# Kernel tuning notes

Hardware: AMD Instinct MI355X
Metric: run time of the kernel (lower is better)

Reference implementation:

```python
import jax, jax.numpy as jnp
import numpy as np

HEADS = 12
HEAD_SIZE = 64
INF = 1e12  # K.infinity() in bert4keras

B, L, D = 8, 1024, 768


def setup_inputs() -> dict:
    key = jax.random.key(0)
    k1, k2 = jax.random.split(key)
    x = jax.random.normal(k1, (B, L, D), dtype=jnp.float32)
    W = jax.random.normal(k2, (D, HEADS * HEAD_SIZE * 2), dtype=jnp.float32) * (1.0 / np.sqrt(D))
    b = jnp.zeros((HEADS * HEAD_SIZE * 2,), dtype=jnp.float32)
    mask = jnp.ones((B, L), dtype=jnp.int32)
    return {"x": x, "W": W, "b": b, "mask": mask}


def _rope_sin_cos(seq_len, head_size, dtype):
    # SinusoidalPositionEmbedding(head_size, 'zero'):
    # emb[n, 2i] = sin(n * 10000^(-2i/S)), emb[n, 2i+1] = cos(...)
    pos = jnp.arange(seq_len, dtype=dtype)                       # [L]
    inv = jnp.power(jnp.asarray(10000.0, dtype),
                    -2.0 * jnp.arange(head_size // 2, dtype=dtype) / head_size)  # [S/2]
    ang = pos[:, None] * inv[None, :]                            # [L, S/2]
    # repeat_elements(..., 2, -1): [c0,c0,c1,c1,...]
    cos_pos = jnp.repeat(jnp.cos(ang), 2, axis=-1)               # [L, S]
    sin_pos = jnp.repeat(jnp.sin(ang), 2, axis=-1)               # [L, S]
    return sin_pos[None, :, None, :], cos_pos[None, :, None, :]  # [1,L,1,S]


def _rotate_half_interleaved(t):
    # stack([-t[...,1::2], t[...,::2]], -1).reshape(t.shape)
    t2 = jnp.stack([-t[..., 1::2], t[..., ::2]], axis=-1)
    return t2.reshape(t.shape)


def reference(x, W, b, mask):
    dtype = x.dtype
    Bq, Lq, _ = x.shape
    S = HEAD_SIZE
    # dense projection + head split: [B, L, H, 2S]
    proj = (jnp.einsum('bld,de->ble', x, W) + b).reshape(Bq, Lq, HEADS, 2 * S)
    qw, kw = proj[..., :S], proj[..., S:]
    # inline RoPE (interleaved variant)
    sin_pos, cos_pos = _rope_sin_cos(Lq, S, dtype)
    qw = qw * cos_pos + _rotate_half_interleaved(qw) * sin_pos
    kw = kw * cos_pos + _rotate_half_interleaved(kw) * sin_pos
    # bilinear score: [B, H, L, L]
    logits = jnp.einsum('bmhd,bnhd->bhmn', qw, kw)
    # padding mask on axis 2 (rows) and axis 3 (cols): x*m + (-INF)*(1-m)
    m = mask.astype(dtype)
    m_row = m[:, None, :, None]
    m_col = m[:, None, None, :]
    logits = logits * m_row + (-INF) * (1.0 - m_row)
    logits = logits * m_col + (-INF) * (1.0 - m_col)
    # upper-triangular (incl. diagonal) mask
    tri = jnp.triu(jnp.ones((Lq, Lq), dtype=dtype))
    logits = logits - (1.0 - tri) * INF
    return logits / np.sqrt(S).astype(np.float32)
```

## Files before the change

kernel.cpp:

```cpp
#include <hip/hip_runtime.h>
#include <hip/hip_bf16.h>
#include <stdint.h>

#define NHEADS 12
#define HS 64
#define NB 8
#define NL 1024
#define ND 768
#define NE 1536
#define INFV 1000000000000.0f

typedef __bf16 bf16x8 __attribute__((ext_vector_type(8)));
typedef float f32x4 __attribute__((ext_vector_type(4)));

typedef __attribute__((address_space(1))) const unsigned int gas_uint;
typedef __attribute__((address_space(3))) unsigned int las_uint;
#define GLOAD_LDS16(g, l) __builtin_amdgcn_global_load_lds((gas_uint*)(g), (las_uint*)(l), 16, 0, 0)

__device__ __forceinline__ unsigned short f2bf(float f) {
  unsigned int u = __builtin_bit_cast(unsigned int, f);
  u += 0x7fffu + ((u >> 16) & 1u);
  return (unsigned short)(u >> 16);
}

__device__ __forceinline__ bf16x8 load_frag(const unsigned short* p) {
  uint4 v = *(const uint4*)p;
  return __builtin_bit_cast(bf16x8, v);
}

__global__ __launch_bounds__(256) void k_prep(
    const float* __restrict__ x, const float* __restrict__ W,
    unsigned short* __restrict__ xb, unsigned short* __restrict__ wt,
    float* __restrict__ cst) {
  const int blk = blockIdx.x;
  if (blk < 6144) {
    int i = blk * 256 + threadIdx.x;
    float4 v = ((const float4*)x)[i];
    ushort4 o;
    o.x = f2bf(v.x); o.y = f2bf(v.y); o.z = f2bf(v.z); o.w = f2bf(v.w);
    ((ushort4*)xb)[i] = o;
  } else if (blk < 6144 + 288) {
    __shared__ float tile[64][65];
    int t = blk - 6144;
    int te = t % 24, td = t / 24;
    int c = threadIdx.x & 63, r4 = threadIdx.x >> 6;
    #pragma unroll
    for (int rr = 0; rr < 16; rr++) {
      int row = rr * 4 + r4;
      tile[row][c] = W[(size_t)(td * 64 + row) * NE + te * 64 + c];
    }
    __syncthreads();
    #pragma unroll
    for (int rr = 0; rr < 16; rr++) {
      int row = rr * 4 + r4;
      wt[(size_t)(te * 64 + row) * ND + td * 64 + c] = f2bf(tile[c][row]);
    }
  } else {
    int t = (blk - 6432) * 256 + threadIdx.x;
    int p = t >> 5, i = t & 31;
    float inv = powf(10000.0f, -(float)i / 32.0f);
    float sv, cv;
    sincosf((float)p * inv, &sv, &cv);
    cst[(p * 32 + i) * 2 + 0] = cv;
    cst[(p * 32 + i) * 2 + 1] = sv;
  }
}

__global__ __launch_bounds__(512, 4) void k_projfill(
    const unsigned short* __restrict__ xb,
    const unsigned short* __restrict__ wt,
    const float* __restrict__ bias,
    const float* __restrict__ cst,
    unsigned short* __restrict__ qbuf, unsigned short* __restrict__ kbuf,
    const int* __restrict__ mask, float* __restrict__ out) {
  __shared__ char smem_b[49152];
  const int tid = threadIdx.x;
  const int blk = blockIdx.x;

  if (blk >= 384) {
    const int e   = blk - 384;
    const int bh  = e / 28;
    int u = e % 28;
    int tm = 1;
    #pragma unroll
    for (int kk = 0; kk < 6; kk++) if (u >= tm) { u -= tm; tm++; }
    const int tn = u;
    const int b  = bh / NHEADS;
    const int* mrow = mask + b * NL;
    const int n0 = tn * 128 + (tid & 31) * 4;
    const int row = tid >> 5;
    int4 mc = *(const int4*)&mrow[n0];
    float o0 = ((mc.x ? 0.0f : -INFV) - INFV) * 0.125f;
    float o1 = ((mc.y ? 0.0f : -INFV) - INFV) * 0.125f;
    float o2 = ((mc.z ? 0.0f : -INFV) - INFV) * 0.125f;
    float o3 = ((mc.w ? 0.0f : -INFV) - INFV) * 0.125f;
    const float oz = (-2.0f * INFV) * 0.125f;
    #pragma unroll
    for (int it = 0; it < 8; it++) {
      int m = tm * 128 + it * 16 + row;
      bool mr1 = (mrow[m] != 0);
      f32x4 o;
      o[0] = mr1 ? o0 : oz;
      o[1] = mr1 ? o1 : oz;
      o[2] = mr1 ? o2 : oz;
      o[3] = mr1 ? o3 : oz;
      __builtin_nontemporal_store(o, (f32x4*)(out + ((size_t)bh * NL + m) * NL + n0));
    }
    return;
  }

  const int xcd = blk & 7;
  const int loc = blk >> 3;
  const int mt  = xcd * 4 + loc / 12;
  const int et  = loc % 12;
  const int m0  = mt * 256;
  const int e0  = et * 128;
  const int lane = tid & 63;
  const int w    = tid >> 6;
  const int wm = w >> 2, wn = w & 3;
  const int col_l = lane & 15, rq = lane >> 4;

  unsigned int goffA[2], goffB[4];
  #pragma unroll
  for (int q = 0; q < 2; q++) {
    int p = q * 512 + tid;
    int r = p >> 3, sl = p & 7;
    goffA[q] = r * ND + (sl ^ (r & 7)) * 8;
  }
  #pragma unroll
  for (int q = 0; q < 4; q++) {
    int p = q * 512 + tid;
    int r = p >> 3, sl = p & 7;
    goffB[q] = r * ND + (sl ^ (r & 7)) * 8;
  }
  const unsigned short* gA = wt + (size_t)e0 * ND;
  const unsigned short* gB = xb + (size_t)m0 * ND;

  const int xr = col_l & 7;
  const unsigned int aRow = (unsigned)((wn * 32 + col_l) * 128);
  const unsigned int bRow = (unsigned)(16384 + (wm * 128 + col_l) * 128);

  f32x4 acc[2][8];
  #pragma unroll
  for (int i = 0; i < 2; i++)
    #pragma unroll
    for (int j = 0; j < 8; j++)
      #pragma unroll
      for (int q = 0; q < 4; q++) acc[i][j][q] = 0.0f;

  for (int kk = 0; kk < ND; kk += 64) {
    const unsigned short* sA = gA + kk;
    const unsigned short* sB = gB + kk;
    #pragma unroll
    for (int q = 0; q < 2; q++) GLOAD_LDS16(sA + goffA[q], smem_b + (q * 512 + tid) * 16);
    #pragma unroll
    for (int q = 0; q < 4; q++) GLOAD_LDS16(sB + goffB[q], smem_b + 16384 + (q * 512 + tid) * 16);
    __syncthreads();
    #pragma unroll
    for (int kkh = 0; kkh < 2; kkh++) {
      const unsigned int so = (((kkh << 2) | rq) ^ xr) * 16;
      bf16x8 af0 = __builtin_bit_cast(bf16x8, *(const uint4*)(smem_b + aRow + 0 * 2048 + so));
      bf16x8 af1 = __builtin_bit_cast(bf16x8, *(const uint4*)(smem_b + aRow + 1 * 2048 + so));
      #pragma unroll
      for (int j = 0; j < 8; j++) {
        bf16x8 bfr = __builtin_bit_cast(bf16x8, *(const uint4*)(smem_b + bRow + j * 2048 + so));
        acc[0][j] = __builtin_amdgcn_mfma_f32_16x16x32_bf16(af0, bfr, acc[0][j], 0, 0, 0);
        acc[1][j] = __builtin_amdgcn_mfma_f32_16x16x32_bf16(af1, bfr, acc[1][j], 0, 0, 0);
      }
    }
    __syncthreads();
  }

  const bool isk = (wn >= 2);
  unsigned short* obuf = isk ? kbuf : qbuf;
  #pragma unroll
  for (int j = 0; j < 8; j++) {
    const int m   = m0 + wm * 128 + j * 16 + col_l;
    const int pos = m & (NL - 1);
    const int bb  = m >> 10;
    const float* crow = cst + pos * 64;
    unsigned short* orow = obuf + (((size_t)(bb * NHEADS + et)) * NL + pos) * HS;
    #pragma unroll
    for (int i = 0; i < 2; i++) {
      const int sl0 = wn * 32 + i * 16 + rq * 4;
      const int s0  = sl0 & 63;
      float4 bv = *(const float4*)&bias[e0 + sl0];
      float4 tq = *(const float4*)(crow + s0);
      float v0 = acc[i][j][0] + bv.x;
      float v1 = acc[i][j][1] + bv.y;
      float v2 = acc[i][j][2] + bv.z;
      float v3 = acc[i][j][3] + bv.w;
      ushort4 o;
      o.x = f2bf(v0 * tq.x - v1 * tq.y);
      o.y = f2bf(v1 * tq.x + v0 * tq.y);
      o.z = f2bf(v2 * tq.z - v3 * tq.w);
      o.w = f2bf(v3 * tq.z + v2 * tq.w);
      *(ushort4*)&orow[s0] = o;
    }
  }
}

__global__ __launch_bounds__(256) void k_logits(
    const unsigned short* __restrict__ qbuf,
    const unsigned short* __restrict__ kbuf,
    const int* __restrict__ mask,
    float* __restrict__ out) {
  const int f  = blockIdx.x;
  const int r  = f & 7, t = f >> 3;
  const int bh = r + 8 * (t / 36);
  int u = t % 36;
  int tm = 0;
  #pragma unroll
  for (int k = 0; k < 7; k++) if (u >= 8 - tm) { u -= 8 - tm; tm++; }
  const int tn = tm + u;
  const int b  = bh / NHEADS;
  const int tid  = threadIdx.x;
  const int* mrow = mask + b * NL;

  const int lane = tid & 63;
  const int w    = tid >> 6;
  const int wm = w >> 1, wn = w & 1;
  const int m_base = tm * 128 + wm * 64;
  const int n_base = tn * 128 + wn * 64;
  const int col_l = lane & 15, rq = lane >> 4;
  const unsigned short* Q = qbuf + (size_t)bh * (NL * HS);
  const unsigned short* K = kbuf + (size_t)bh * (NL * HS);

  __shared__ float lds[64 * 128];

  f32x4 acc[4][4];
  #pragma unroll
  for (int i = 0; i < 4; i++)
    #pragma unroll
    for (int j = 0; j < 4; j++)
      #pragma unroll
      for (int q = 0; q < 4; q++) acc[i][j][q] = 0.0f;

  #pragma unroll
  for (int ks = 0; ks < 2; ks++) {
    bf16x8 ak[4], bq[4];
    #pragma unroll
    for (int ff = 0; ff < 4; ff++) {
      ak[ff] = load_frag(K + (size_t)(n_base + ff * 16 + col_l) * HS + ks * 32 + rq * 8);
      bq[ff] = load_frag(Q + (size_t)(m_base + ff * 16 + col_l) * HS + ks * 32 + rq * 8);
    }
    #pragma unroll
    for (int i = 0; i < 4; i++)
      #pragma unroll
      for (int j = 0; j < 4; j++)
        acc[i][j] = __builtin_amdgcn_mfma_f32_16x16x32_bf16(ak[i], bq[j], acc[i][j], 0, 0, 0);
  }

  const bool diag = (tn == tm);
  const int rb_row = tid >> 5;
  const int rb_c4  = (tid & 31) * 4;
  const int n_rb   = tn * 128 + rb_c4;
  int4 mc_rb = *(const int4*)&mrow[n_rb];
  const bool allmc = (mc_rb.x & mc_rb.y & mc_rb.z & mc_rb.w) != 0;

  #pragma unroll
  for (int pass = 0; pass < 2; pass++) {
    if (wm == pass) {
      #pragma unroll
      for (int j = 0; j < 4; j++) {
        const int rl = j * 16 + col_l;
        const int sw = (rl & 7) << 2;
        #pragma unroll
        for (int i = 0; i < 4; i++) {
          const int c = (wn * 64 + i * 16 + rq * 4) ^ sw;
          *(f32x4*)&lds[rl * 128 + c] = acc[i][j];
        }
      }
    }
    __syncthreads();
    #pragma unroll
    for (int it = 0; it < 8; it++) {
      const int rl = it * 8 + rb_row;
      const int m  = tm * 128 + pass * 64 + rl;
      const int c  = rb_c4 ^ ((rl & 7) << 2);
      f32x4 v = *(const f32x4*)&lds[rl * 128 + c];
      if (mrow[m] == 0) { v[0] = -INFV; v[1] = -INFV; v[2] = -INFV; v[3] = -INFV; }
      if (!allmc) {
        if (mc_rb.x == 0) v[0] = -INFV;
        if (mc_rb.y == 0) v[1] = -INFV;
        if (mc_rb.z == 0) v[2] = -INFV;
        if (mc_rb.w == 0) v[3] = -INFV;
      }
      if (diag) {
        if (n_rb + 0 < m) v[0] -= INFV;
        if (n_rb + 1 < m) v[1] -= INFV;
        if (n_rb + 2 < m) v[2] -= INFV;
        if (n_rb + 3 < m) v[3] -= INFV;
      }
      v *= 0.125f;
      __builtin_nontemporal_store(v, (f32x4*)(out + ((size_t)bh * NL + m) * NL + n_rb));
    }
    __syncthreads();
  }
}

extern "C" void kernel_launch(void* const* d_in, const int* in_sizes, int n_in,
                              void* d_out, int out_size, void* d_ws, size_t ws_size,
                              hipStream_t stream) {
  const float* x    = (const float*)d_in[0];
  const float* W    = (const float*)d_in[1];
  const float* bias = (const float*)d_in[2];
  const int*   mask = (const int*)d_in[3];
  float* out = (float*)d_out;
  char* ws = (char*)d_ws;

  unsigned short* xb = (unsigned short*)(ws);
  unsigned short* wt = (unsigned short*)(ws + 12582912);
  unsigned short* qb = (unsigned short*)(ws + 14942208);
  unsigned short* kb = (unsigned short*)(ws + 27525120);
  float* cst = (float*)(ws + 40108032);

  k_prep<<<6560, 256, 0, stream>>>(x, W, xb, wt, cst);
  k_projfill<<<384 + 2688, 512, 0, stream>>>(xb, wt, bias, cst, qb, kb, mask, out);
  k_logits<<<3456, 256, 0, stream>>>(qb, kb, mask, out);
}
```

Measured before the change: 119.9 us.

## Fuse projection and logits kernels with per-head atomic flag dependencies

Merges the projection/fill kernel and the logits kernel into one launch. Projection blocks release a per-(batch, head) counter after writing Q/K, and logits blocks (two 256-thread tiles per 512-thread block) spin on that counter before computing. This removes the kernel boundary and lets logits work overlap with projection and the fill stores. It adds a memset, spin-waits, and a forward-progress risk if waiting blocks occupy the CUs before the producers are scheduled. Doubled LDS per block may also lower occupancy.

Result: slower. 135.4 us (+13.0%).

```diff
diff --git a/kernel.cpp b/kernel.cpp
--- a/kernel.cpp
+++ b/kernel.cpp
@@ -66,18 +66,116 @@
   }
 }
 
-__global__ __launch_bounds__(512, 4) void k_projfill(
+__global__ __launch_bounds__(512, 4) void k_fused(
     const unsigned short* __restrict__ xb,
     const unsigned short* __restrict__ wt,
     const float* __restrict__ bias,
     const float* __restrict__ cst,
     unsigned short* __restrict__ qbuf, unsigned short* __restrict__ kbuf,
-    const int* __restrict__ mask, float* __restrict__ out) {
-  __shared__ char smem_b[49152];
+    const int* __restrict__ mask, float* __restrict__ out,
+    int* __restrict__ flags) {
+  __shared__ char smem_b[65536];
   const int tid = threadIdx.x;
   const int blk = blockIdx.x;
 
-  if (blk >= 384) {
+  if (blk < 384) {
+    const int xcd = blk & 7;
+    const int loc = blk >> 3;
+    const int mt  = xcd * 4 + loc / 12;
+    const int et  = loc % 12;
+    const int m0  = mt * 256;
+    const int e0  = et * 128;
+    const int lane = tid & 63;
+    const int w    = tid >> 6;
+    const int wm = w >> 2, wn = w & 3;
+    const int col_l = lane & 15, rq = lane >> 4;
+
+    unsigned int goffA[2], goffB[4];
+    #pragma unroll
+    for (int q = 0; q < 2; q++) {
+      int p = q * 512 + tid;
+      int r = p >> 3, sl = p & 7;
+      goffA[q] = r * ND + (sl ^ (r & 7)) * 8;
+    }
+    #pragma unroll
+    for (int q = 0; q < 4; q++) {
+      int p = q * 512 + tid;
+      int r = p >> 3, sl = p & 7;
+      goffB[q] = r * ND + (sl ^ (r & 7)) * 8;
+    }
+    const unsigned short* gA = wt + (size_t)e0 * ND;
+    const unsigned short* gB = xb + (size_t)m0 * ND;
+
+    const int xr = col_l & 7;
+    const unsigned int aRow = (unsigned)((wn * 32 + col_l) * 128);
+    const unsigned int bRow = (unsigned)(16384 + (wm * 128 + col_l) * 128);
+
+    f32x4 acc[2][8];
+    #pragma unroll
+    for (int i = 0; i < 2; i++)
+      #pragma unroll
+      for (int j = 0; j < 8; j++)
+        #pragma unroll
+        for (int q = 0; q < 4; q++) acc[i][j][q] = 0.0f;
+
+    for (int kk = 0; kk < ND; kk += 64) {
+      const unsigned short* sA = gA + kk;
+      const unsigned short* sB = gB + kk;
+      #pragma unroll
+      for (int q = 0; q < 2; q++) GLOAD_LDS16(sA + goffA[q], smem_b + (q * 512 + tid) * 16);
+      #pragma unroll
+      for (int q = 0; q < 4; q++) GLOAD_LDS16(sB + goffB[q], smem_b + 16384 + (q * 512 + tid) * 16);
+      __syncthreads();
+      #pragma unroll
+      for (int kkh = 0; kkh < 2; kkh++) {
+        const unsigned int so = (((kkh << 2) | rq) ^ xr) * 16;
+        bf16x8 af0 = __builtin_bit_cast(bf16x8, *(const uint4*)(smem_b + aRow + 0 * 2048 + so));
+        bf16x8 af1 = __builtin_bit_cast(bf16x8, *(const uint4*)(smem_b + aRow + 1 * 2048 + so));
+        #pragma unroll
+        for (int j = 0; j < 8; j++) {
+          bf16x8 bfr = __builtin_bit_cast(bf16x8, *(const uint4*)(smem_b + bRow + j * 2048 + so));
+          acc[0][j] = __builtin_amdgcn_mfma_f32_16x16x32_bf16(af0, bfr, acc[0][j], 0, 0, 0);
+          acc[1][j] = __builtin_amdgcn_mfma_f32_16x16x32_bf16(af1, bfr, acc[1][j], 0, 0, 0);
+        }
+      }
+      __syncthreads();
+    }
+
+    const bool isk = (wn >= 2);
+    unsigned short* obuf = isk ? kbuf : qbuf;
+    #pragma unroll
+    for (int j = 0; j < 8; j++) {
+      const int m   = m0 + wm * 128 + j * 16 + col_l;
+      const int pos = m & (NL - 1);
+      const int bb  = m >> 10;
+      const float* crow = cst + pos * 64;
+      unsigned short* orow = obuf + (((size_t)(bb * NHEADS + et)) * NL + pos) * HS;
+      #pragma unroll
+      for (int i = 0; i < 2; i++) {
+        const int sl0 = wn * 32 + i * 16 + rq * 4;
+        const int s0  = sl0 & 63;
+        float4 bv = *(const float4*)&bias[e0 + sl0];
+        float4 tq = *(const float4*)(crow + s0);
+        float v0 = acc[i][j][0] + bv.x;
+        float v1 = acc[i][j][1] + bv.y;
+        float v2 = acc[i][j][2] + bv.z;
+        float v3 = acc[i][j][3] + bv.w;
+        ushort4 o;
+        o.x = f2bf(v0 * tq.x - v1 * tq.y);
+        o.y = f2bf(v1 * tq.x + v0 * tq.y);
+        o.z = f2bf(v2 * tq.z - v3 * tq.w);
+        o.w = f2bf(v3 * tq.z + v2 * tq.w);
+        *(ushort4*)&orow[s0] = o;
+      }
+    }
+    __syncthreads();
+    if (tid == 0)
+      __hip_atomic_fetch_add(&flags[(mt >> 2) * 12 + et], 1,
+                             __ATOMIC_RELEASE, __HIP_MEMORY_SCOPE_AGENT);
+    return;
+  }
+
+  if (blk < 3072) {
     const int e   = blk - 384;
     const int bh  = e / 28;
     int u = e % 28;
@@ -109,193 +207,108 @@
     return;
   }
 
-  const int xcd = blk & 7;
-  const int loc = blk >> 3;
-  const int mt  = xcd * 4 + loc / 12;
-  const int et  = loc % 12;
-  const int m0  = mt * 256;
-  const int e0  = et * 128;
-  const int lane = tid & 63;
-  const int w    = tid >> 6;
-  const int wm = w >> 2, wn = w & 3;
-  const int col_l = lane & 15, rq = lane >> 4;
-
-  unsigned int goffA[2], goffB[4];
-  #pragma unroll
-  for (int q = 0; q < 2; q++) {
-    int p = q * 512 + tid;
-    int r = p >> 3, sl = p & 7;
-    goffA[q] = r * ND + (sl ^ (r & 7)) * 8;
-  }
-  #pragma unroll
-  for (int q = 0; q < 4; q++) {
-    int p = q * 512 + tid;
-    int r = p >> 3, sl = p & 7;
-    goffB[q] = r * ND + (sl ^ (r & 7)) * 8;
-  }
-  const unsigned short* gA = wt + (size_t)e0 * ND;
-  const unsigned short* gB = xb + (size_t)m0 * ND;
-
-  const int xr = col_l & 7;
-  const unsigned int aRow = (unsigned)((wn * 32 + col_l) * 128);
-  const unsigned int bRow = (unsigned)(16384 + (wm * 128 + col_l) * 128);
-
-  f32x4 acc[2][8];
-  #pragma unroll
-  for (int i = 0; i < 2; i++)
-    #pragma unroll
-    for (int j = 0; j < 8; j++)
-      #pragma unroll
-      for (int q = 0; q < 4; q++) acc[i][j][q] = 0.0f;
-
-  for (int kk = 0; kk < ND; kk += 64) {
-    const unsigned short* sA = gA + kk;
-    const unsigned short* sB = gB + kk;
-    #pragma unroll
-    for (int q = 0; q < 2; q++) GLOAD_LDS16(sA + goffA[q], smem_b + (q * 512 + tid) * 16);
-    #pragma unroll
-    for (int q = 0; q < 4; q++) GLOAD_LDS16(sB + goffB[q], smem_b + 16384 + (q * 512 + tid) * 16);
+  {
+    const int q_ = blk - 3072;
+    const int r  = q_ & 7;
+    const int tt = q_ >> 3;
+    const int sub = tid >> 8;
+    const int tl  = tid & 255;
+    const int t  = tt * 2 + sub;
+    const int bh = r + 8 * (t / 36);
+    int u = t % 36;
+    int tm = 0;
+    #pragma unroll
+    for (int k = 0; k < 7; k++) if (u >= 8 - tm) { u -= 8 - tm; tm++; }
+    const int tn = tm + u;
+    const int b  = bh / NHEADS;
+    const int* mrow = mask + b * NL;
+
+    if (tl == 0) {
+      while (__hip_atomic_load(&flags[bh], __ATOMIC_ACQUIRE,
+                               __HIP_MEMORY_SCOPE_AGENT) < 4)
+        __builtin_amdgcn_s_sleep(8);
+    }
     __syncthreads();
-    #pragma unroll
-    for (int kkh = 0; kkh < 2; kkh++) {
-      const unsigned int so = (((kkh << 2) | rq) ^ xr) * 16;
-      bf16x8 af0 = __builtin_bit_cast(bf16x8, *(const uint4*)(smem_b + aRow + 0 * 2048 + so));
-      bf16x8 af1 = __builtin_bit_cast(bf16x8, *(const uint4*)(smem_b + aRow + 1 * 2048 + so));
-      #pragma unroll
-      for (int j = 0; j < 8; j++) {
-        bf16x8 bfr = __builtin_bit_cast(bf16x8, *(const uint4*)(smem_b + bRow + j * 2048 + so));
-        acc[0][j] = __builtin_amdgcn_mfma_f32_16x16x32_bf16(af0, bfr, acc[0][j], 0, 0, 0);
-        acc[1][j] = __builtin_amdgcn_mfma_f32_16x16x32_bf16(af1, bfr, acc[1][j], 0, 0, 0);
-      }
-    }
-    __syncthreads();
-  }
-
-  const bool isk = (wn >= 2);
-  unsigned short* obuf = isk ? kbuf : qbuf;
-  #pragma unroll
-  for (int j = 0; j < 8; j++) {
-    const int m   = m0 + wm * 128 + j * 16 + col_l;
-    const int pos = m & (NL - 1);
-    const int bb  = m >> 10;
-    const float* crow = cst + pos * 64;
-    unsigned short* orow = obuf + (((size_t)(bb * NHEADS + et)) * NL + pos) * HS;
-    #pragma unroll
-    for (int i = 0; i < 2; i++) {
-      const int sl0 = wn * 32 + i * 16 + rq * 4;
-      const int s0  = sl0 & 63;
-      float4 bv = *(const float4*)&bias[e0 + sl0];
-      float4 tq = *(const float4*)(crow + s0);
-      float v0 = acc[i][j][0] + bv.x;
-      float v1 = acc[i][j][1] + bv.y;
-      float v2 = acc[i][j][2] + bv.z;
-      float v3 = acc[i][j][3] + bv.w;
-      ushort4 o;
-      o.x = f2bf(v0 * tq.x - v1 * tq.y);
-      o.y = f2bf(v1 * tq.x + v0 * tq.y);
-      o.z = f2bf(v2 * tq.z - v3 * tq.w);
-      o.w = f2bf(v3 * tq.z + v2 * tq.w);
-      *(ushort4*)&orow[s0] = o;
-    }
-  }
-}
-
-__global__ __launch_bounds__(256) void k_logits(
-    const unsigned short* __restrict__ qbuf,
-    const unsigned short* __restrict__ kbuf,
-    const int* __restrict__ mask,
-    float* __restrict__ out) {
-  const int f  = blockIdx.x;
-  const int r  = f & 7, t = f >> 3;
-  const int bh = r + 8 * (t / 36);
-  int u = t % 36;
-  int tm = 0;
-  #pragma unroll
-  for (int k = 0; k < 7; k++) if (u >= 8 - tm) { u -= 8 - tm; tm++; }
-  const int tn = tm + u;
-  const int b  = bh / NHEADS;
-  const int tid  = threadIdx.x;
-  const int* mrow = mask + b * NL;
-
-  const int lane = tid & 63;
-  const int w    = tid >> 6;
-  const int wm = w >> 1, wn = w & 1;
-  const int m_base = tm * 128 + wm * 64;
-  const int n_base = tn * 128 + wn * 64;
-  const int col_l = lane & 15, rq = lane >> 4;
-  const unsigned short* Q = qbuf + (size_t)bh * (NL * HS);
-  const unsigned short* K = kbuf + (size_t)bh * (NL * HS);
-
-  __shared__ float lds[64 * 128];
-
-  f32x4 acc[4][4];
-  #pragma unroll
-  for (int i = 0; i < 4; i++)
-    #pragma unroll
-    for (int j = 0; j < 4; j++)
-      #pragma unroll
-      for (int q = 0; q < 4; q++) acc[i][j][q] = 0.0f;
-
-  #pragma unroll
-  for (int ks = 0; ks < 2; ks++) {
-    bf16x8 ak[4], bq[4];
-    #pragma unroll
-    for (int ff = 0; ff < 4; ff++) {
-      ak[ff] = load_frag(K + (size_t)(n_base + ff * 16 + col_l) * HS + ks * 32 + rq * 8);
-      bq[ff] = load_frag(Q + (size_t)(m_base + ff * 16 + col_l) * HS + ks * 32 + rq * 8);
-    }
+
+    const int lane = tl & 63;
+    const int w    = tl >> 6;
+    const int wm = w >> 1, wn = w & 1;
+    const int m_base = tm * 128 + wm * 64;
+    const int n_base = tn * 128 + wn * 64;
+    const int col_l = lane & 15, rq = lane >> 4;
+    const unsigned short* Q = qbuf + (size_t)bh * (NL * HS);
+    const unsigned short* K = kbuf + (size_t)bh * (NL * HS);
+    float* lds = (float*)(smem_b + sub * 32768);
+
+    f32x4 acc[4][4];
     #pragma unroll
     for (int i = 0; i < 4; i++)
       #pragma unroll
       for (int j = 0; j < 4; j++)
-        acc[i][j] = __builtin_amdgcn_mfma_f32_16x16x32_bf16(ak[i], bq[j], acc[i][j], 0, 0, 0);
-  }
-
-  const bool diag = (tn == tm);
-  const int rb_row = tid >> 5;
-  const int rb_c4  = (tid & 31) * 4;
-  const int n_rb   = tn * 128 + rb_c4;
-  int4 mc_rb = *(const int4*)&mrow[n_rb];
-  const bool allmc = (mc_rb.x & mc_rb.y & mc_rb.z & mc_rb.w) != 0;
-
-  #pragma unroll
-  for (int pass = 0; pass < 2; pass++) {
-    if (wm == pass) {
-      #pragma unroll
-      for (int j = 0; j < 4; j++) {
-        const int rl = j * 16 + col_l;
-        const int sw = (rl & 7) << 2;
-        #pragma unroll
-        for (int i = 0; i < 4; i++) {
-          const int c = (wn * 64 + i * 16 + rq * 4) ^ sw;
-          *(f32x4*)&lds[rl * 128 + c] = acc[i][j];
+        #pragma unroll
+        for (int q = 0; q < 4; q++) acc[i][j][q] = 0.0f;
+
+    #pragma unroll
+    for (int ks = 0; ks < 2; ks++) {
+      bf16x8 ak[4], bq[4];
+      #pragma unroll
+      for (int ff = 0; ff < 4; ff++) {
+        ak[ff] = load_frag(K + (size_t)(n_base + ff * 16 + col_l) * HS + ks * 32 + rq * 8);
+        bq[ff] = load_frag(Q + (size_t)(m_base + ff * 16 + col_l) * HS + ks * 32 + rq * 8);
+      }
+      #pragma unroll
+      for (int i = 0; i < 4; i++)
+        #pragma unroll
+        for (int j = 0; j < 4; j++)
+          acc[i][j] = __builtin_amdgcn_mfma_f32_16x16x32_bf16(ak[i], bq[j], acc[i][j], 0, 0, 0);
+    }
+
+    const bool diag = (tn == tm);
+    const int rb_row = tl >> 5;
+    const int rb_c4  = (tl & 31) * 4;
+    const int n_rb   = tn * 128 + rb_c4;
+    int4 mc_rb = *(const int4*)&mrow[n_rb];
+    const bool allmc = (mc_rb.x & mc_rb.y & mc_rb.z & mc_rb.w) != 0;
+
+    #pragma unroll
+    for (int pass = 0; pass < 2; pass++) {
+      if (wm == pass) {
+        #pragma unroll
+        for (int j = 0; j < 4; j++) {
+          const int rl = j * 16 + col_l;
+          const int sw = (rl & 7) << 2;
+          #pragma unroll
+          for (int i = 0; i < 4; i++) {
+            const int c = (wn * 64 + i * 16 + rq * 4) ^ sw;
+            *(f32x4*)&lds[rl * 128 + c] = acc[i][j];
+          }
         }
       }
-    }
-    __syncthreads();
-    #pragma unroll
-    for (int it = 0; it < 8; it++) {
-      const int rl = it * 8 + rb_row;
-      const int m  = tm * 128 + pass * 64 + rl;
-      const int c  = rb_c4 ^ ((rl & 7) << 2);
-      f32x4 v = *(const f32x4*)&lds[rl * 128 + c];
-      if (mrow[m] == 0) { v[0] = -INFV; v[1] = -INFV; v[2] = -INFV; v[3] = -INFV; }
-      if (!allmc) {
-        if (mc_rb.x == 0) v[0] = -INFV;
-        if (mc_rb.y == 0) v[1] = -INFV;
-        if (mc_rb.z == 0) v[2] = -INFV;
-        if (mc_rb.w == 0) v[3] = -INFV;
-      }
-      if (diag) {
-        if (n_rb + 0 < m) v[0] -= INFV;
-        if (n_rb + 1 < m) v[1] -= INFV;
-        if (n_rb + 2 < m) v[2] -= INFV;
-        if (n_rb + 3 < m) v[3] -= INFV;
-      }
-      v *= 0.125f;
-      __builtin_nontemporal_store(v, (f32x4*)(out + ((size_t)bh * NL + m) * NL + n_rb));
-    }
-    __syncthreads();
+      __syncthreads();
+      #pragma unroll
+      for (int it = 0; it < 8; it++) {
+        const int rl = it * 8 + rb_row;
+        const int m  = tm * 128 + pass * 64 + rl;
+        const int c  = rb_c4 ^ ((rl & 7) << 2);
+        f32x4 v = *(const f32x4*)&lds[rl * 128 + c];
+        if (mrow[m] == 0) { v[0] = -INFV; v[1] = -INFV; v[2] = -INFV; v[3] = -INFV; }
+        if (!allmc) {
+          if (mc_rb.x == 0) v[0] = -INFV;
+          if (mc_rb.y == 0) v[1] = -INFV;
+          if (mc_rb.z == 0) v[2] = -INFV;
+          if (mc_rb.w == 0) v[3] = -INFV;
+        }
+        if (diag) {
+          if (n_rb + 0 < m) v[0] -= INFV;
+          if (n_rb + 1 < m) v[1] -= INFV;
+          if (n_rb + 2 < m) v[2] -= INFV;
+          if (n_rb + 3 < m) v[3] -= INFV;
+        }
+        v *= 0.125f;
+        __builtin_nontemporal_store(v, (f32x4*)(out + ((size_t)bh * NL + m) * NL + n_rb));
+      }
+      __syncthreads();
+    }
   }
 }
 
@@ -314,8 +327,9 @@
   unsigned short* qb = (unsigned short*)(ws + 14942208);
   unsigned short* kb = (unsigned short*)(ws + 27525120);
   float* cst = (float*)(ws + 40108032);
-
+  int* flags = (int*)(ws + 40370176);
+
+  hipMemsetAsync(flags, 0, 96 * sizeof(int), stream);
   k_prep<<<6560, 256, 0, stream>>>(x, W, xb, wt, cst);
-  k_projfill<<<384 + 2688, 512, 0, stream>>>(xb, wt, bias, cst, qb, kb, mask, out);
-  k_logits<<<3456, 256, 0, stream>>>(qb, kb, mask, out);
-}
+  k_fused<<<4800, 512, 0, stream>>>(xb, wt, bias, cst, qb, kb, mask, out, flags);
+}
```
